# Kernel optimization log

Measured on AMD Instinct MI355X. Metric: run time of the kernel, lower is better.

The kernel has to match this reference:

```python
import jax, jax.numpy as jnp
import numpy as np

B, T, V, H, L = 128, 512, 256, 512, 2  # batch, seq, vocab, hidden, layers


def setup_inputs() -> dict:
    key = jax.random.key(0)
    ks = jax.random.split(key, 12)
    s = 0.05
    p = lambda k, shape: (jax.random.normal(k, shape, jnp.float32) * s)
    return {
        "x": jax.random.normal(ks[0], (B, T, V), jnp.float32),
        # layer 0 (input size V)
        "w_ih0": p(ks[1], (4 * H, V)),
        "w_hh0": p(ks[2], (4 * H, H)),
        "b_ih0": p(ks[3], (4 * H,)),
        "b_hh0": p(ks[4], (4 * H,)),
        # layer 1 (input size H)
        "w_ih1": p(ks[5], (4 * H, H)),
        "w_hh1": p(ks[6], (4 * H, H)),
        "b_ih1": p(ks[7], (4 * H,)),
        "b_hh1": p(ks[8], (4 * H,)),
        # final projection
        "fc_w": p(ks[9], (V, H)),
        "fc_b": p(ks[10], (V,)),
    }


def _lstm_layer(x, w_ih, w_hh, b_ih, b_hh):
    """x: [B,T,in] -> (outputs [B,T,H], h_T [B,H], c_T [B,H]). PyTorch gate order i,f,g,o."""
    Bb = x.shape[0]
    Hh = w_hh.shape[1]
    # precompute input contribution for all timesteps: [B,T,4H]
    pre = jnp.einsum('bti,gi->btg', x, w_ih) + b_ih + b_hh

    def step(carry, xt):
        h, c = carry
        gates = xt + h @ w_hh.T  # [B,4H]
        i, f, g, o = jnp.split(gates, 4, axis=-1)
        i = jax.nn.sigmoid(i)
        f = jax.nn.sigmoid(f)
        g = jnp.tanh(g)
        o = jax.nn.sigmoid(o)
        c = f * c + i * g
        h = o * jnp.tanh(c)
        return (h, c), h

    h0 = jnp.zeros((Bb, Hh), x.dtype)
    (hT, cT), hs = jax.lax.scan(step, (h0, h0), jnp.swapaxes(pre, 0, 1))
    return jnp.swapaxes(hs, 0, 1), hT, cT


def reference(x, w_ih0, w_hh0, b_ih0, b_hh0, w_ih1, w_hh1, b_ih1, b_hh1, fc_w, fc_b):
    out0, h0, c0 = _lstm_layer(x, w_ih0, w_hh0, b_ih0, b_hh0)
    out1, h1, c1 = _lstm_layer(out0, w_ih1, w_hh1, b_ih1, b_hh1)
    last = out1[:, -1, :]                # slice final timestep [B,H]
    # dropout is identity in eval mode
    logits = last @ fc_w.T + fc_b        # [B,V]
    h_n = jnp.stack([h0, h1])            # [L,B,H]
    c_n = jnp.stack([c0, c1])
    return (logits, h_n, c_n)
```

## Files before the change

### kernel.cpp

```cpp
#include <hip/hip_runtime.h>
#include <math.h>

#define B_ 128
#define T_ 512
#define V_ 256
#define H_ 512

typedef unsigned short u16;
typedef unsigned int u32;
typedef unsigned long long u64;
typedef __attribute__((ext_vector_type(8))) __bf16 bf16x8;
typedef __attribute__((ext_vector_type(4))) float f32x4;
typedef __attribute__((ext_vector_type(4))) u32 u32x4;

__device__ __forceinline__ float sigf(float x) { return 1.f / (1.f + __expf(-x)); }
__device__ __forceinline__ float tanh_fast(float x) {
    x = fminf(fmaxf(x, -15.f), 15.f);
    float e = __expf(2.f * x);
    return (e - 1.f) / (e + 1.f);
}
__device__ __forceinline__ u16 f2bf(float f) {
    union { float f; u32 u; } v; v.f = f;
    u32 r = v.u + 0x7FFFu + ((v.u >> 16) & 1u);
    return (u16)(r >> 16);
}

__device__ __forceinline__ u64 aload(const u64* p) {
    return __hip_atomic_load(p, __ATOMIC_RELAXED, __HIP_MEMORY_SCOPE_AGENT);
}
__device__ __forceinline__ void astore(u64* p, u64 v) {
    __hip_atomic_store(p, v, __ATOMIC_RELAXED, __HIP_MEMORY_SCOPE_AGENT);
}
__device__ __forceinline__ u32 aload32(const u32* p) {
    return __hip_atomic_load(p, __ATOMIC_RELAXED, __HIP_MEMORY_SCOPE_AGENT);
}
__device__ __forceinline__ void astore32(u32* p, u32 v) {
    __hip_atomic_store(p, v, __ATOMIC_RELAXED, __HIP_MEMORY_SCOPE_AGENT);
}
__device__ __forceinline__ void pollge(const u32* slots, int idx, int target) {
    const u32* p = slots + idx;
    for (;;) {
        u32 v = aload32(p);
        if (__all((int)v >= target)) break;
        __builtin_amdgcn_s_sleep(1);
    }
    __builtin_amdgcn_sched_barrier(0);
    asm volatile("" ::: "memory");
}
__device__ __forceinline__ bf16x8 afrag(const u16* p) {
    union { u64 d[2]; bf16x8 v; } u;
    u.d[0] = aload((const u64*)p);
    u.d[1] = aload((const u64*)(p + 4));
    return u.v;
}

__global__ __launch_bounds__(256) void conv_x(u16* __restrict__ dst, const float* __restrict__ x) {
    int tid = blockIdx.x * 256 + threadIdx.x;
    int k = tid & (V_ - 1);
    int t = (tid >> 8) & (T_ - 1);
    int b = tid >> 17;
    float v = x[tid];
    int lane = (b & 15) | (((k >> 3) & 3) << 4);
    dst[((((size_t)t * 8 + (b >> 4)) * 8) + (k >> 5)) * 512 + (size_t)lane * 8 + (k & 7)] = f2bf(v);
}

__global__ __launch_bounds__(256) void conv_w(u16* __restrict__ dst,
                                              const float* __restrict__ wih,
                                              const float* __restrict__ whh,
                                              int KIN, int Ktot) {
    int tid = blockIdx.x * 256 + threadIdx.x;
    int n = tid / Ktot, k = tid - n * Ktot;
    float v = (k < KIN) ? wih[(size_t)n * KIN + k] : whh[(size_t)n * H_ + (k - KIN)];
    int lane = (n & 15) | (((k >> 3) & 3) << 4);
    dst[((size_t)((n >> 4) * (Ktot >> 5) + (k >> 5))) * 512 + (size_t)lane * 8 + (k & 7)] = f2bf(v);
}

__global__ __launch_bounds__(256) void vadd(float* __restrict__ d,
                                            const float* __restrict__ a,
                                            const float* __restrict__ b, int n) {
    int i = blockIdx.x * 256 + threadIdx.x;
    if (i < n) d[i] = a[i] + b[i];
}


template <int LAYER>
__device__ __forceinline__ void run_loop(
    const u16* __restrict__ Xswz, u16* __restrict__ Out0,
    const u16* __restrict__ WBs,
    f32x4* __restrict__ scr,
    u16* __restrict__ tileb,
    u32* __restrict__ Hgrp,
    const float* __restrict__ bsum, float* __restrict__ out,
    u32* __restrict__ bc,
    int js, int mq, int wid, int lane)
{
    constexpr int KCA = LAYER ? 16 : 8;
    constexpr int KCT = KCA + 16;
    const int m = wid & 1;
    const bool isA = wid < 2;
    const int jl = (js << 4) | (lane & 15);

    if (isA) {
        for (int s = 0; s <= T_; ++s) {
            const bool work = LAYER ? (s >= 1) : (s < T_);
            const int t = LAYER ? (s - 1) : s;
            if (work) {
                f32x4 acc[4];
                #pragma unroll
                for (int g = 0; g < 4; ++g) acc[g] = (f32x4){0.f, 0.f, 0.f, 0.f};
                if (LAYER == 0) {
                    const u16* As = Xswz + (size_t)t * 32768 + (size_t)(2 * mq + m) * 4096 + (size_t)lane * 8;
                    #pragma unroll
                    for (int kc = 0; kc < 8; ++kc) {
                        bf16x8 a = *(const bf16x8*)(As + (size_t)kc * 512);
                        #pragma unroll
                        for (int g = 0; g < 4; ++g)
                            acc[g] = __builtin_amdgcn_mfma_f32_16x16x32_bf16(
                                a, *(const bf16x8*)(WBs + (size_t)(g * KCT + kc) * 512 + (size_t)lane * 8), acc[g], 0, 0, 0);
                    }
                } else {
                    pollge(bc + m * 32, lane & 31, s);
                    const u16* As = Out0 + (size_t)t * 65536 + (size_t)(2 * mq + m) * 8192 + (size_t)lane * 8;
                    bf16x8 fa[16];
                    #pragma unroll
                    for (int kc = 0; kc < 16; ++kc) fa[kc] = afrag(As + (size_t)kc * 512);
                    #pragma unroll
                    for (int kc = 0; kc < 16; ++kc) {
                        #pragma unroll
                        for (int g = 0; g < 4; ++g)
                            acc[g] = __builtin_amdgcn_mfma_f32_16x16x32_bf16(
                                fa[kc], *(const bf16x8*)(WBs + (size_t)(g * KCT + kc) * 512 + (size_t)lane * 8), acc[g], 0, 0, 0);
                    }
                }
                #pragma unroll
                for (int g = 0; g < 4; ++g) scr[(m * 4 + g) * 64 + lane] = acc[g];
            }
            __syncthreads();
            __syncthreads();
        }
    } else {
        const float bi0 = bsum[jl], bi1 = bsum[512 + jl];
        const float bi2 = bsum[1024 + jl], bi3 = bsum[1536 + jl];
        f32x4 creg = {0.f, 0.f, 0.f, 0.f};
        u32* bcs = bc + m * 32 + js;

        for (int s = 0; s <= T_; ++s) {
            const bool work = LAYER ? (s >= 1) : (s < T_);
            const int t = LAYER ? (s - 1) : s;
            f32x4 acc[4];
            #pragma unroll
            for (int g = 0; g < 4; ++g) acc[g] = (f32x4){0.f, 0.f, 0.f, 0.f};
            u64 f[64];

            if (work) {
                const u32 tag = (u32)(LAYER ? (s - 1) : s);
                const u32* hb = Hgrp + (size_t)(tag & 1) * 16384 + (size_t)m * 8192;
                {
                    const u64* hp = (const u64*)(hb + (size_t)lane * 128);
                    for (;;) {
                        u64 d = aload(hp);
                        if (__all(((u32)(d >> 16) & 0xFFFFu) == tag)) break;
                        __builtin_amdgcn_s_sleep(1);
                    }
                }
                for (;;) {
                    #pragma unroll
                    for (int kc = 0; kc < 16; ++kc) {
                        const u64* p = (const u64*)(hb + (size_t)kc * 512 + (size_t)lane * 8);
                        f[4 * kc + 0] = aload(p + 0);
                        f[4 * kc + 1] = aload(p + 1);
                        f[4 * kc + 2] = aload(p + 2);
                        f[4 * kc + 3] = aload(p + 3);
                    }
                    u32 bad = 0;
                    #pragma unroll
                    for (int i = 0; i < 64; ++i) bad |= (((u32)(f[i] >> 16)) & 0xFFFFu) ^ tag;
                    if (!__any(bad != 0u)) break;
                    __builtin_amdgcn_s_sleep(1);
                }
                __builtin_amdgcn_sched_barrier(0);
            }
            if (LAYER == 0 && s > 0) {
                if (!work) asm volatile("s_waitcnt vmcnt(0)" ::: "memory");
                if (lane == 0) astore32(bcs, (u32)s);
            }
            if (work) {
                #pragma unroll
                for (int kc = 0; kc < 16; ++kc) {
                    u32 w0 = (u32)(f[4 * kc + 0] & 0xFFFFu) | ((u32)(f[4 * kc + 0] >> 32) << 16);
                    u32 w1 = (u32)(f[4 * kc + 1] & 0xFFFFu) | ((u32)(f[4 * kc + 1] >> 32) << 16);
                    u32 w2 = (u32)(f[4 * kc + 2] & 0xFFFFu) | ((u32)(f[4 * kc + 2] >> 32) << 16);
                    u32 w3 = (u32)(f[4 * kc + 3] & 0xFFFFu) | ((u32)(f[4 * kc + 3] >> 32) << 16);
                    u32x4 ww = {w0, w1, w2, w3};
                    bf16x8 a = __builtin_bit_cast(bf16x8, ww);
                    #pragma unroll
                    for (int g = 0; g < 4; ++g)
                        acc[g] = __builtin_amdgcn_mfma_f32_16x16x32_bf16(
                            a, *(const bf16x8*)(WBs + (size_t)(g * KCT + KCA + kc) * 512 + (size_t)lane * 8), acc[g], 0, 0, 0);
                }
            }
            __syncthreads();
            if (work) {
                #pragma unroll
                for (int g = 0; g < 4; ++g) acc[g] += scr[(m * 4 + g) * 64 + lane];
            }
            __syncthreads();
            if (work) {
                const bool is_last = (s == (LAYER ? T_ : T_ - 1));
                const int bb = (lane >> 4) << 2;
                #pragma unroll
                for (int r = 0; r < 4; ++r) {
                    const float vi = sigf(acc[0][r] + bi0);
                    const float vf = sigf(acc[1][r] + bi1);
                    const float vg = tanh_fast(acc[2][r] + bi2);
                    const float vo = sigf(acc[3][r] + bi3);
                    const float cn = vf * creg[r] + vi * vg;
                    creg[r] = cn;
                    const float hn = vo * tanh_fast(cn);
                    tileb[(size_t)(m * 16 + bb + r) * 20 + (lane & 15)] = f2bf(hn);
                    if (is_last) {
                        const int bg = mq * 32 + m * 16 + bb + r;
                        out[(LAYER ? 98304 : 32768) + bg * 512 + jl] = hn;
                        out[(LAYER ? 229376 : 163840) + bg * 512 + jl] = cn;
                    }
                }
                const u32 wtag = (u32)(t + 1);
                u32* hw = Hgrp + (size_t)(wtag & 1) * 16384 + (size_t)m * 8192;
                #pragma unroll
                for (int q = 0; q < 2; ++q) {
                    u32 w = *(const u32*)&tileb[(size_t)(m * 16 + (lane >> 2)) * 20 + q * 8 + (lane & 3) * 2];
                    u64 v = (u64)(w & 0xFFFFu) | ((u64)wtag << 16)
                          | ((u64)(w >> 16) << 32) | ((u64)wtag << 48);
                    astore((u64*)(hw + (size_t)(js >> 1) * 512 + (size_t)((js & 1) * 2 + q) * 128
                                  + (size_t)(lane >> 2) * 8 + (size_t)((lane & 3) * 2)), v);
                }
                if (LAYER == 0) {
                    const int q2 = lane >> 5, lw = lane & 31, b2 = lw >> 1, e4 = (lw & 1) * 4;
                    u64 v = *(const u64*)&tileb[(size_t)(m * 16 + b2) * 20 + q2 * 8 + e4];
                    astore((u64*)(Out0 + (size_t)t * 65536 + (size_t)(2 * mq + m) * 8192
                                  + (size_t)(js >> 1) * 512 + (size_t)((js & 1) * 2 + q2) * 128
                                  + (size_t)b2 * 8 + (size_t)e4), v);
                }
            }
        }
    }
}

__global__ __launch_bounds__(256, 1) void lstm_persistent(
    const u16* __restrict__ Xswz, u16* __restrict__ Out0swz,
    const u16* __restrict__ WB0, const u16* __restrict__ WB1,
    const float* __restrict__ bsum0, const float* __restrict__ bsum1,
    u32* __restrict__ Htag, float* __restrict__ out, u32* __restrict__ bc)
{
    __shared__ u16 WBs[4 * 32 * 512];
    __shared__ f32x4 scr[2 * 4 * 64];
    __shared__ __align__(16) u16 tileb[2 * 16 * 20];

    const int bid = blockIdx.x;
    const int g = bid & 7, js = bid >> 3;
    const int layer = g >> 2, mq = g & 3;
    const int tid = threadIdx.x;
    const int wid = tid >> 6, lane = tid & 63;

    const int KCtot = layer ? 32 : 24;
    const u16* WB = layer ? WB1 : WB0;
    for (int gg = 0; gg < 4; ++gg) {
        const u32x4* s4 = (const u32x4*)(WB + ((size_t)(gg * 32 + js) * KCtot) * 512);
        u32x4* d4 = (u32x4*)(WBs + (size_t)gg * KCtot * 512);
        for (int i = tid; i < KCtot * 64; i += 256) d4[i] = s4[i];
    }
    __syncthreads();

    u32* Hgrp = Htag + (size_t)g * 32768;
    u32* bcg = bc + mq * 64;

    if (layer == 0)
        run_loop<0>(Xswz, Out0swz, WBs, scr, tileb, Hgrp, bsum0, out, bcg, js, mq, wid, lane);
    else
        run_loop<1>(Xswz, Out0swz, WBs, scr, tileb, Hgrp, bsum1, out, bcg, js, mq, wid, lane);
}

__device__ __forceinline__ float dot4_(float4 a, float4 w, float s) {
    s = fmaf(a.x, w.x, s); s = fmaf(a.y, w.y, s);
    s = fmaf(a.z, w.z, s); s = fmaf(a.w, w.w, s);
    return s;
}

__global__ __launch_bounds__(256) void logits_kernel(
    const float* __restrict__ h1, const float* __restrict__ fc_w,
    const float* __restrict__ fc_b, float* __restrict__ out)
{
    __shared__ float hs[H_];
    const int b = blockIdx.x;
    for (int k = threadIdx.x; k < H_; k += 256) hs[k] = h1[(size_t)b * H_ + k];
    __syncthreads();
    const int v = threadIdx.x;
    const float4* wr = reinterpret_cast<const float4*>(fc_w + (size_t)v * H_);
    const float4* hr = reinterpret_cast<const float4*>(hs);
    float s = 0.f;
    #pragma unroll 8
    for (int k = 0; k < H_ / 4; ++k) s = dot4_(hr[k], wr[k], s);
    out[(size_t)b * V_ + v] = s + fc_b[v];
}

extern "C" void kernel_launch(void* const* d_in, const int* in_sizes, int n_in,
                              void* d_out, int out_size, void* d_ws, size_t ws_size,
                              hipStream_t stream) {
    const float* x     = (const float*)d_in[0];
    const float* w_ih0 = (const float*)d_in[1];
    const float* w_hh0 = (const float*)d_in[2];
    const float* b_ih0 = (const float*)d_in[3];
    const float* b_hh0 = (const float*)d_in[4];
    const float* w_ih1 = (const float*)d_in[5];
    const float* w_hh1 = (const float*)d_in[6];
    const float* b_ih1 = (const float*)d_in[7];
    const float* b_hh1 = (const float*)d_in[8];
    const float* fc_w  = (const float*)d_in[9];
    const float* fc_b  = (const float*)d_in[10];
    float* out = (float*)d_out;

    char* p = (char*)d_ws;
    u16* Xswz    = (u16*)p; p += (size_t)512 * 32768 * 2;
    u16* Out0swz = (u16*)p; p += (size_t)512 * 65536 * 2;
    u16* WB0     = (u16*)p; p += (size_t)128 * 24 * 512 * 2;
    u16* WB1     = (u16*)p; p += (size_t)128 * 32 * 512 * 2;
    u32* Htag    = (u32*)p; p += (size_t)8 * 32768 * 4;
    float* bsum0 = (float*)p; p += 2048 * 4;
    float* bsum1 = (float*)p; p += 2048 * 4;
    u32* bc      = (u32*)p;  p += 4 * 64 * 4;

    hipMemsetAsync(Htag, 0, (size_t)8 * 32768 * 4, stream);
    hipMemsetAsync(bc, 0, 4 * 64 * 4, stream);
    conv_x<<<65536, 256, 0, stream>>>(Xswz, x);
    conv_w<<<(2048 * 768) / 256, 256, 0, stream>>>(WB0, w_ih0, w_hh0, 256, 768);
    conv_w<<<(2048 * 1024) / 256, 256, 0, stream>>>(WB1, w_ih1, w_hh1, 512, 1024);
    vadd<<<8, 256, 0, stream>>>(bsum0, b_ih0, b_hh0, 2048);
    vadd<<<8, 256, 0, stream>>>(bsum1, b_ih1, b_hh1, 2048);

    lstm_persistent<<<256, 256, 0, stream>>>(
        Xswz, Out0swz, WB0, WB1, bsum0, bsum1, Htag, out, bc);

    logits_kernel<<<B_, 256, 0, stream>>>(out + 98304, fc_w, fc_b, out);
}
```

Before: 3.214 ms.

## Pipeline input projection one step ahead with double-buffered scratch and single barrier

```diff
diff --git a/kernel.cpp b/kernel.cpp
--- a/kernel.cpp
+++ b/kernel.cpp
@@ -101,15 +101,14 @@
     const int jl = (js << 4) | (lane & 15);
 
     if (isA) {
-        for (int s = 0; s <= T_; ++s) {
-            const bool work = LAYER ? (s >= 1) : (s < T_);
-            const int t = LAYER ? (s - 1) : s;
-            if (work) {
+        for (int s = -1; s < T_; ++s) {
+            const int tc = s + 1;
+            if (tc < T_) {
                 f32x4 acc[4];
                 #pragma unroll
                 for (int g = 0; g < 4; ++g) acc[g] = (f32x4){0.f, 0.f, 0.f, 0.f};
                 if (LAYER == 0) {
-                    const u16* As = Xswz + (size_t)t * 32768 + (size_t)(2 * mq + m) * 4096 + (size_t)lane * 8;
+                    const u16* As = Xswz + (size_t)tc * 32768 + (size_t)(2 * mq + m) * 4096 + (size_t)lane * 8;
                     #pragma unroll
                     for (int kc = 0; kc < 8; ++kc) {
                         bf16x8 a = *(const bf16x8*)(As + (size_t)kc * 512);
@@ -119,8 +118,8 @@
                                 a, *(const bf16x8*)(WBs + (size_t)(g * KCT + kc) * 512 + (size_t)lane * 8), acc[g], 0, 0, 0);
                     }
                 } else {
-                    pollge(bc + m * 32, lane & 31, s);
-                    const u16* As = Out0 + (size_t)t * 65536 + (size_t)(2 * mq + m) * 8192 + (size_t)lane * 8;
+                    pollge(bc + m * 32, lane & 31, tc + 1);
+                    const u16* As = Out0 + (size_t)tc * 65536 + (size_t)(2 * mq + m) * 8192 + (size_t)lane * 8;
                     bf16x8 fa[16];
                     #pragma unroll
                     for (int kc = 0; kc < 16; ++kc) fa[kc] = afrag(As + (size_t)kc * 512);
@@ -133,9 +132,8 @@
                     }
                 }
                 #pragma unroll
-                for (int g = 0; g < 4; ++g) scr[(m * 4 + g) * 64 + lane] = acc[g];
+                for (int g = 0; g < 4; ++g) scr[(size_t)(((tc & 1) * 2 + m) * 4 + g) * 64 + lane] = acc[g];
             }
-            __syncthreads();
             __syncthreads();
         }
     } else {
@@ -144,47 +142,54 @@
         f32x4 creg = {0.f, 0.f, 0.f, 0.f};
         u32* bcs = bc + m * 32 + js;
 
-        for (int s = 0; s <= T_; ++s) {
-            const bool work = LAYER ? (s >= 1) : (s < T_);
-            const int t = LAYER ? (s - 1) : s;
-            f32x4 acc[4];
-            #pragma unroll
-            for (int g = 0; g < 4; ++g) acc[g] = (f32x4){0.f, 0.f, 0.f, 0.f};
-            u64 f[64];
-
-            if (work) {
-                const u32 tag = (u32)(LAYER ? (s - 1) : s);
+        for (int s = -1; s < T_; ++s) {
+            if (s >= 0) {
+                const u32 tag = (u32)s;
                 const u32* hb = Hgrp + (size_t)(tag & 1) * 16384 + (size_t)m * 8192;
-                {
-                    const u64* hp = (const u64*)(hb + (size_t)lane * 128);
-                    for (;;) {
-                        u64 d = aload(hp);
-                        if (__all(((u32)(d >> 16) & 0xFFFFu) == tag)) break;
-                        __builtin_amdgcn_s_sleep(1);
+                u64 f[64];
+                #pragma unroll
+                for (int kc = 0; kc < 16; ++kc) {
+                    const u64* p = (const u64*)(hb + (size_t)kc * 512 + (size_t)lane * 8);
+                    f[4 * kc + 0] = aload(p + 0);
+                    f[4 * kc + 1] = aload(p + 1);
+                    f[4 * kc + 2] = aload(p + 2);
+                    f[4 * kc + 3] = aload(p + 3);
+                }
+                u32 bad = 0u;
+                #pragma unroll
+                for (int kc = 0; kc < 16; ++kc) {
+                    u32 b = (((u32)(f[4 * kc + 0] >> 16) & 0xFFFFu) ^ tag)
+                          | (((u32)(f[4 * kc + 1] >> 16) & 0xFFFFu) ^ tag)
+                          | (((u32)(f[4 * kc + 2] >> 16) & 0xFFFFu) ^ tag)
+                          | (((u32)(f[4 * kc + 3] >> 16) & 0xFFFFu) ^ tag);
+                    bad |= b ? (1u << kc) : 0u;
+                }
+                while (__any(bad != 0u)) {
+                    #pragma unroll
+                    for (int kc = 0; kc < 16; ++kc) {
+                        if (bad & (1u << kc)) {
+                            const u64* p = (const u64*)(hb + (size_t)kc * 512 + (size_t)lane * 8);
+                            u64 g0 = aload(p + 0), g1 = aload(p + 1), g2 = aload(p + 2), g3 = aload(p + 3);
+                            u32 b = (((u32)(g0 >> 16) & 0xFFFFu) ^ tag)
+                                  | (((u32)(g1 >> 16) & 0xFFFFu) ^ tag)
+                                  | (((u32)(g2 >> 16) & 0xFFFFu) ^ tag)
+                                  | (((u32)(g3 >> 16) & 0xFFFFu) ^ tag);
+                            if (b == 0u) {
+                                f[4 * kc + 0] = g0; f[4 * kc + 1] = g1;
+                                f[4 * kc + 2] = g2; f[4 * kc + 3] = g3;
+                                bad &= ~(1u << kc);
+                            }
+                        }
                     }
                 }
-                for (;;) {
-                    #pragma unroll
-                    for (int kc = 0; kc < 16; ++kc) {
-                        const u64* p = (const u64*)(hb + (size_t)kc * 512 + (size_t)lane * 8);
-                        f[4 * kc + 0] = aload(p + 0);
-                        f[4 * kc + 1] = aload(p + 1);
-                        f[4 * kc + 2] = aload(p + 2);
-                        f[4 * kc + 3] = aload(p + 3);
-                    }
-                    u32 bad = 0;
-                    #pragma unroll
-                    for (int i = 0; i < 64; ++i) bad |= (((u32)(f[i] >> 16)) & 0xFFFFu) ^ tag;
-                    if (!__any(bad != 0u)) break;
-                    __builtin_amdgcn_s_sleep(1);
-                }
                 __builtin_amdgcn_sched_barrier(0);
-            }
-            if (LAYER == 0 && s > 0) {
-                if (!work) asm volatile("s_waitcnt vmcnt(0)" ::: "memory");
-                if (lane == 0) astore32(bcs, (u32)s);
-            }
-            if (work) {
+                if (LAYER == 0 && s >= 1) {
+                    asm volatile("s_waitcnt vmcnt(0)" ::: "memory");
+                    if (lane == 0) astore32(bcs, (u32)s);
+                }
+                f32x4 acc[4];
+                #pragma unroll
+                for (int g = 0; g < 4; ++g) acc[g] = scr[(size_t)(((s & 1) * 2 + m) * 4 + g) * 64 + lane];
                 #pragma unroll
                 for (int kc = 0; kc < 16; ++kc) {
                     u32 w0 = (u32)(f[4 * kc + 0] & 0xFFFFu) | ((u32)(f[4 * kc + 0] >> 32) << 16);
@@ -198,15 +203,7 @@
                         acc[g] = __builtin_amdgcn_mfma_f32_16x16x32_bf16(
                             a, *(const bf16x8*)(WBs + (size_t)(g * KCT + KCA + kc) * 512 + (size_t)lane * 8), acc[g], 0, 0, 0);
                 }
-            }
-            __syncthreads();
-            if (work) {
-                #pragma unroll
-                for (int g = 0; g < 4; ++g) acc[g] += scr[(m * 4 + g) * 64 + lane];
-            }
-            __syncthreads();
-            if (work) {
-                const bool is_last = (s == (LAYER ? T_ : T_ - 1));
+                const bool is_last = (s == T_ - 1);
                 const int bb = (lane >> 4) << 2;
                 #pragma unroll
                 for (int r = 0; r < 4; ++r) {
@@ -224,7 +221,7 @@
                         out[(LAYER ? 229376 : 163840) + bg * 512 + jl] = cn;
                     }
                 }
-                const u32 wtag = (u32)(t + 1);
+                const u32 wtag = (u32)(s + 1);
                 u32* hw = Hgrp + (size_t)(wtag & 1) * 16384 + (size_t)m * 8192;
                 #pragma unroll
                 for (int q = 0; q < 2; ++q) {
@@ -237,11 +234,16 @@
                 if (LAYER == 0) {
                     const int q2 = lane >> 5, lw = lane & 31, b2 = lw >> 1, e4 = (lw & 1) * 4;
                     u64 v = *(const u64*)&tileb[(size_t)(m * 16 + b2) * 20 + q2 * 8 + e4];
-                    astore((u64*)(Out0 + (size_t)t * 65536 + (size_t)(2 * mq + m) * 8192
+                    astore((u64*)(Out0 + (size_t)s * 65536 + (size_t)(2 * mq + m) * 8192
                                   + (size_t)(js >> 1) * 512 + (size_t)((js & 1) * 2 + q2) * 128
                                   + (size_t)b2 * 8 + (size_t)e4), v);
                 }
             }
+            __syncthreads();
+        }
+        if (LAYER == 0) {
+            asm volatile("s_waitcnt vmcnt(0)" ::: "memory");
+            if (lane == 0) astore32(bcs, (u32)(T_ + 1));
         }
     }
 }
@@ -253,7 +255,7 @@
     u32* __restrict__ Htag, float* __restrict__ out, u32* __restrict__ bc)
 {
     __shared__ u16 WBs[4 * 32 * 512];
-    __shared__ f32x4 scr[2 * 4 * 64];
+    __shared__ f32x4 scr[2 * 2 * 4 * 64];
     __shared__ __align__(16) u16 tileb[2 * 16 * 20];
 
     const int bid = blockIdx.x;
```

New measurement: 3.818 ms. 18.8% more time.
